# Kernel optimization log

Measured on AMD Instinct MI355X. Metric: run time of the kernel, lower is better.

The kernel has to match this reference:

```python
import jax, jax.numpy as jnp
import numpy as np

N_IN, N_OUT = 8192, 4096
INIT_TAU = 2.0
V_TH = 1.0
SLOPE = 10.0  # fast-sigmoid surrogate slope


def setup_inputs() -> dict:
    key = jax.random.key(0)
    k1, k2, k3, k4, k5 = jax.random.split(key, 5)
    x = jax.random.normal(k1, (N_IN,), jnp.float32)
    W = jax.random.normal(k2, (N_IN, N_OUT), jnp.float32) / np.sqrt(N_IN).astype(np.float32)
    u = jax.random.normal(k3, (N_OUT,), jnp.float32)
    E = jax.random.normal(k4, (N_IN, N_OUT), jnp.float32) * 0.1
    R_hat = jax.random.normal(k5, (N_IN, N_OUT), jnp.float32) * 0.1
    g_bar = jnp.zeros((N_OUT,), jnp.float32)
    ratio = jnp.zeros((1,), jnp.float32)
    return {"x": x, "W": W, "u": u, "E": E, "R_hat": R_hat, "g_bar": g_bar, "ratio": ratio}


def _step(x, W, u, E, R_hat, g_bar, ratio):
    # One OTPE timestep. SNN: Dense connection + LIF with soft (detached) reset.
    sig_tau = jax.nn.sigmoid(jnp.float32(INIT_TAU))
    u_pre = sig_tau * u + x @ W                       # [n_out]
    s = (u_pre >= V_TH).astype(jnp.float32)           # spike (heaviside fwd)
    sg = 1.0 / (1.0 + SLOPE * jnp.abs(u_pre - V_TH)) ** 2  # surrogate d s/d u_pre
    u_new = u_pre - s * V_TH                          # soft reset (s detached)
    # analytic per-step VJPs of sum(s) and sum(u) wrt (u_prev, theta):
    ds_du_prev = sg * sig_tau                         # [n_out]
    ds_dtheta_cur = x[:, None] * sg[None, :]          # [n_in, n_out]
    # du_cur_du_prev = sig_tau ; du_cur_dtheta_cur = outer(x, ones)
    ds_dtheta = ds_du_prev[None, :] * E + ds_dtheta_cur   # map_s over pytree
    E_new = sig_tau * E + x[:, None]                      # map_u over pytree
    R_new = sig_tau * R_hat + ds_dtheta                   # map_r
    r0 = sig_tau * ratio                               # [1]
    ratio_new = r0 + 1.0
    r = r0 / ratio_new
    g_bar_new = r * g_bar + (1.0 - r) * (ds_du_prev / sig_tau)
    return s, u_new, E_new, R_new, g_bar_new, ratio_new


def reference(x, W, u, E, R_hat, g_bar, ratio):
    # returns (s, carry_u, carry_E, carry_R_hat, carry_g_bar, carry_ratio)
    return _step(x, W, u, E, R_hat, g_bar, ratio)
```

## Files before the change

kernel.cpp:

```cpp
#include <hip/hip_runtime.h>


#define SIG_TAU 0.8807970779778823f

typedef float f32x4 __attribute__((ext_vector_type(4)));

constexpr int N_IN  = 8192;
constexpr int N_OUT = 4096;
constexpr int NCG   = N_OUT / 4;
constexpr int NCHUNK = 256;
constexpr int ROWS_PER_CHUNK = N_IN / NCHUNK;
constexpr int ROWS_PER_CHUNK_ATOM = 64;

constexpr size_t OFF_S     = 0;
constexpr size_t OFF_U     = (size_t)N_OUT;
constexpr size_t OFF_E     = (size_t)2 * N_OUT;
constexpr size_t OFF_R     = OFF_E + (size_t)N_IN * N_OUT;
constexpr size_t OFF_G     = OFF_R + (size_t)N_IN * N_OUT;
constexpr size_t OFF_RATIO = OFF_G + (size_t)N_OUT;

__global__ __launch_bounds__(256) void matvec_split(
    const float* __restrict__ x, const f32x4* __restrict__ W4,
    f32x4* __restrict__ part4) {
    const int cg    = blockIdx.x * 256 + threadIdx.x;
    const int chunk = blockIdx.y;
    const int row0  = chunk * ROWS_PER_CHUNK;
    f32x4 a = {0.f, 0.f, 0.f, 0.f};
#pragma unroll 8
    for (int r = 0; r < ROWS_PER_CHUNK; ++r) {
        const float xv = x[row0 + r];
        const f32x4 w  = __builtin_nontemporal_load(
            &W4[(size_t)(row0 + r) * NCG + cg]);
        a[0] = fmaf(xv, w[0], a[0]);
        a[1] = fmaf(xv, w[1], a[1]);
        a[2] = fmaf(xv, w[2], a[2]);
        a[3] = fmaf(xv, w[3], a[3]);
    }
    part4[(size_t)chunk * NCG + cg] = a;
}

__global__ __launch_bounds__(256) void matvec_atomic(
    const float* __restrict__ x, const f32x4* __restrict__ W4,
    float* __restrict__ acc) {
    const int cg   = blockIdx.x * 256 + threadIdx.x;
    const int row0 = blockIdx.y * ROWS_PER_CHUNK_ATOM;
    f32x4 a = {0.f, 0.f, 0.f, 0.f};
#pragma unroll 8
    for (int r = 0; r < ROWS_PER_CHUNK_ATOM; ++r) {
        const float xv = x[row0 + r];
        const f32x4 w  = W4[(size_t)(row0 + r) * NCG + cg];
        a[0] = fmaf(xv, w[0], a[0]);
        a[1] = fmaf(xv, w[1], a[1]);
        a[2] = fmaf(xv, w[2], a[2]);
        a[3] = fmaf(xv, w[3], a[3]);
    }
    float* dst = acc + (size_t)cg * 4;
    atomicAdd(dst + 0, a[0]);
    atomicAdd(dst + 1, a[1]);
    atomicAdd(dst + 2, a[2]);
    atomicAdd(dst + 3, a[3]);
}

__global__ __launch_bounds__(256) void finalize(
    const float* __restrict__ part, const int nchunks,
    const float* __restrict__ u, const float* __restrict__ g_bar,
    const float* __restrict__ ratio, float* __restrict__ out,
    float* __restrict__ sg_ws) {
    const int j = blockIdx.x * 256 + threadIdx.x;
    if (j >= N_OUT) return;
    float acc = 0.f;
#pragma unroll 8
    for (int c = 0; c < nchunks; ++c)
        acc += part[(size_t)c * N_OUT + j];

    const float u_pre = fmaf(SIG_TAU, u[j], acc);
    const float s     = (u_pre >= 1.0f) ? 1.0f : 0.0f;
    const float t     = 1.0f / fmaf(10.0f, fabsf(u_pre - 1.0f), 1.0f);
    const float sg    = t * t;
    const float u_new = u_pre - s;

    const float r0        = SIG_TAU * ratio[0];
    const float ratio_new = r0 + 1.0f;
    const float r         = r0 / ratio_new;
    const float g_new = fmaf(r, g_bar[j], (1.0f - r) * sg);

    out[OFF_S + j] = s;
    out[OFF_U + j] = u_new;
    out[OFF_G + j] = g_new;
    sg_ws[j] = sg;
    if (j == 0) out[OFF_RATIO] = ratio_new;
}

__global__ __launch_bounds__(256) void elemwise(
    const float* __restrict__ x, const f32x4* __restrict__ E4,
    const f32x4* __restrict__ R4, const f32x4* __restrict__ sg4,
    f32x4* __restrict__ Enew4, f32x4* __restrict__ Rnew4) {
    const int tid = threadIdx.x;
    const f32x4 s0 = sg4[tid];
    const f32x4 s1 = sg4[tid + 256];
    const f32x4 s2 = sg4[tid + 512];
    const f32x4 s3 = sg4[tid + 768];

    for (int row = blockIdx.x; row < N_IN; row += gridDim.x) {
        const float  xv   = x[row];
        const size_t base = (size_t)row * NCG + tid;

        const f32x4 e0 = E4[base];
        const f32x4 e1 = E4[base + 256];
        const f32x4 e2 = E4[base + 512];
        const f32x4 e3 = E4[base + 768];
        const f32x4 r0 = R4[base];
        const f32x4 r1 = R4[base + 256];
        const f32x4 r2 = R4[base + 512];
        const f32x4 r3 = R4[base + 768];

        f32x4 en0, en1, en2, en3, rn0, rn1, rn2, rn3;
#define COMP(k)                                                   \
        en##k[0] = fmaf(SIG_TAU, e##k[0], xv);                    \
        en##k[1] = fmaf(SIG_TAU, e##k[1], xv);                    \
        en##k[2] = fmaf(SIG_TAU, e##k[2], xv);                    \
        en##k[3] = fmaf(SIG_TAU, e##k[3], xv);                    \
        rn##k[0] = fmaf(s##k[0], en##k[0], SIG_TAU * r##k[0]);    \
        rn##k[1] = fmaf(s##k[1], en##k[1], SIG_TAU * r##k[1]);    \
        rn##k[2] = fmaf(s##k[2], en##k[2], SIG_TAU * r##k[2]);    \
        rn##k[3] = fmaf(s##k[3], en##k[3], SIG_TAU * r##k[3]);
        COMP(0) COMP(1) COMP(2) COMP(3)
#undef COMP

        Enew4[base]       = en0;
        Enew4[base + 256] = en1;
        Enew4[base + 512] = en2;
        Enew4[base + 768] = en3;
        Rnew4[base]       = rn0;
        Rnew4[base + 256] = rn1;
        Rnew4[base + 512] = rn2;
        Rnew4[base + 768] = rn3;
    }
}

extern "C" void kernel_launch(void* const* d_in, const int* in_sizes, int n_in,
                              void* d_out, int out_size, void* d_ws, size_t ws_size,
                              hipStream_t stream) {
    const float* x     = (const float*)d_in[0];
    const float* W     = (const float*)d_in[1];
    const float* u     = (const float*)d_in[2];
    const float* E     = (const float*)d_in[3];
    const float* R_hat = (const float*)d_in[4];
    const float* g_bar = (const float*)d_in[5];
    const float* ratio = (const float*)d_in[6];
    float* out = (float*)d_out;

    float* sg   = (float*)d_ws;
    float* part = sg + N_OUT;

    const size_t need = (size_t)(N_OUT + (size_t)NCHUNK * N_OUT) * sizeof(float);
    if (ws_size >= need) {
        dim3 g1(NCG / 256, NCHUNK);
        matvec_split<<<g1, 256, 0, stream>>>(x, (const f32x4*)W, (f32x4*)part);
        finalize<<<N_OUT / 256, 256, 0, stream>>>(
            part, NCHUNK, u, g_bar, ratio, out, sg);
    } else {
        hipMemsetAsync(part, 0, N_OUT * sizeof(float), stream);
        dim3 g1(NCG / 256, N_IN / ROWS_PER_CHUNK_ATOM);
        matvec_atomic<<<g1, 256, 0, stream>>>(x, (const f32x4*)W, part);
        finalize<<<N_OUT / 256, 256, 0, stream>>>(
            part, 1, u, g_bar, ratio, out, sg);
    }

    elemwise<<<2048, 256, 0, stream>>>(
        x, (const f32x4*)E, (const f32x4*)R_hat, (const f32x4*)sg,
        (f32x4*)(out + OFF_E), (f32x4*)(out + OFF_R));
}
```

Baseline: 538.7 us.

## Split elementwise kernel into E update before finalize and R update after

Splits the fused E/R update into two kernels: E_new is computed right after the matvec, before finalize, since it does not depend on the surrogate gradient. The R kernel then reads E_new back from the output instead of recomputing it. Nontemporal loads and stores are added on the streaming arrays. This adds an extra full-size read of E_new and relies on same-stream ordering, so no true overlap is gained.

Measured after the change: 530.2 us. No clear change (-1.6%).

```diff
diff --git a/kernel.cpp b/kernel.cpp
--- a/kernel.cpp
+++ b/kernel.cpp
@@ -91,50 +91,62 @@
     if (j == 0) out[OFF_RATIO] = ratio_new;
 }
 
-__global__ __launch_bounds__(256) void elemwise(
+__global__ __launch_bounds__(256) void ew_E(
     const float* __restrict__ x, const f32x4* __restrict__ E4,
-    const f32x4* __restrict__ R4, const f32x4* __restrict__ sg4,
-    f32x4* __restrict__ Enew4, f32x4* __restrict__ Rnew4) {
+    f32x4* __restrict__ Enew4) {
+    const int tid = threadIdx.x;
+    for (int row = blockIdx.x; row < N_IN; row += gridDim.x) {
+        const float  xv   = x[row];
+        const size_t base = (size_t)row * NCG + tid;
+        const f32x4 e0 = __builtin_nontemporal_load(&E4[base]);
+        const f32x4 e1 = __builtin_nontemporal_load(&E4[base + 256]);
+        const f32x4 e2 = __builtin_nontemporal_load(&E4[base + 512]);
+        const f32x4 e3 = __builtin_nontemporal_load(&E4[base + 768]);
+        f32x4 en0, en1, en2, en3;
+#define CE(k)                                      \
+        en##k[0] = fmaf(SIG_TAU, e##k[0], xv);     \
+        en##k[1] = fmaf(SIG_TAU, e##k[1], xv);     \
+        en##k[2] = fmaf(SIG_TAU, e##k[2], xv);     \
+        en##k[3] = fmaf(SIG_TAU, e##k[3], xv);
+        CE(0) CE(1) CE(2) CE(3)
+#undef CE
+        Enew4[base]       = en0;
+        Enew4[base + 256] = en1;
+        Enew4[base + 512] = en2;
+        Enew4[base + 768] = en3;
+    }
+}
+
+__global__ __launch_bounds__(256) void ew_R(
+    const f32x4* __restrict__ R4, const f32x4* __restrict__ Enew4,
+    const f32x4* __restrict__ sg4, f32x4* __restrict__ Rnew4) {
     const int tid = threadIdx.x;
     const f32x4 s0 = sg4[tid];
     const f32x4 s1 = sg4[tid + 256];
     const f32x4 s2 = sg4[tid + 512];
     const f32x4 s3 = sg4[tid + 768];
-
     for (int row = blockIdx.x; row < N_IN; row += gridDim.x) {
-        const float  xv   = x[row];
         const size_t base = (size_t)row * NCG + tid;
-
-        const f32x4 e0 = E4[base];
-        const f32x4 e1 = E4[base + 256];
-        const f32x4 e2 = E4[base + 512];
-        const f32x4 e3 = E4[base + 768];
-        const f32x4 r0 = R4[base];
-        const f32x4 r1 = R4[base + 256];
-        const f32x4 r2 = R4[base + 512];
-        const f32x4 r3 = R4[base + 768];
-
-        f32x4 en0, en1, en2, en3, rn0, rn1, rn2, rn3;
-#define COMP(k)                                                   \
-        en##k[0] = fmaf(SIG_TAU, e##k[0], xv);                    \
-        en##k[1] = fmaf(SIG_TAU, e##k[1], xv);                    \
-        en##k[2] = fmaf(SIG_TAU, e##k[2], xv);                    \
-        en##k[3] = fmaf(SIG_TAU, e##k[3], xv);                    \
+        const f32x4 r0 = __builtin_nontemporal_load(&R4[base]);
+        const f32x4 r1 = __builtin_nontemporal_load(&R4[base + 256]);
+        const f32x4 r2 = __builtin_nontemporal_load(&R4[base + 512]);
+        const f32x4 r3 = __builtin_nontemporal_load(&R4[base + 768]);
+        const f32x4 en0 = Enew4[base];
+        const f32x4 en1 = Enew4[base + 256];
+        const f32x4 en2 = Enew4[base + 512];
+        const f32x4 en3 = Enew4[base + 768];
+        f32x4 rn0, rn1, rn2, rn3;
+#define CR(k)                                                     \
         rn##k[0] = fmaf(s##k[0], en##k[0], SIG_TAU * r##k[0]);    \
         rn##k[1] = fmaf(s##k[1], en##k[1], SIG_TAU * r##k[1]);    \
         rn##k[2] = fmaf(s##k[2], en##k[2], SIG_TAU * r##k[2]);    \
         rn##k[3] = fmaf(s##k[3], en##k[3], SIG_TAU * r##k[3]);
-        COMP(0) COMP(1) COMP(2) COMP(3)
-#undef COMP
-
-        Enew4[base]       = en0;
-        Enew4[base + 256] = en1;
-        Enew4[base + 512] = en2;
-        Enew4[base + 768] = en3;
-        Rnew4[base]       = rn0;
-        Rnew4[base + 256] = rn1;
-        Rnew4[base + 512] = rn2;
-        Rnew4[base + 768] = rn3;
+        CR(0) CR(1) CR(2) CR(3)
+#undef CR
+        __builtin_nontemporal_store(rn0, &Rnew4[base]);
+        __builtin_nontemporal_store(rn1, &Rnew4[base + 256]);
+        __builtin_nontemporal_store(rn2, &Rnew4[base + 512]);
+        __builtin_nontemporal_store(rn3, &Rnew4[base + 768]);
     }
 }
 
@@ -153,21 +165,25 @@
     float* sg   = (float*)d_ws;
     float* part = sg + N_OUT;
 
+    f32x4* Enew4 = (f32x4*)(out + OFF_E);
+    f32x4* Rnew4 = (f32x4*)(out + OFF_R);
+
     const size_t need = (size_t)(N_OUT + (size_t)NCHUNK * N_OUT) * sizeof(float);
     if (ws_size >= need) {
         dim3 g1(NCG / 256, NCHUNK);
         matvec_split<<<g1, 256, 0, stream>>>(x, (const f32x4*)W, (f32x4*)part);
+        ew_E<<<2048, 256, 0, stream>>>(x, (const f32x4*)E, Enew4);
         finalize<<<N_OUT / 256, 256, 0, stream>>>(
             part, NCHUNK, u, g_bar, ratio, out, sg);
     } else {
         hipMemsetAsync(part, 0, N_OUT * sizeof(float), stream);
         dim3 g1(NCG / 256, N_IN / ROWS_PER_CHUNK_ATOM);
         matvec_atomic<<<g1, 256, 0, stream>>>(x, (const f32x4*)W, part);
+        ew_E<<<2048, 256, 0, stream>>>(x, (const f32x4*)E, Enew4);
         finalize<<<N_OUT / 256, 256, 0, stream>>>(
             part, 1, u, g_bar, ratio, out, sg);
     }
 
-    elemwise<<<2048, 256, 0, stream>>>(
-        x, (const f32x4*)E, (const f32x4*)R_hat, (const f32x4*)sg,
-        (f32x4*)(out + OFF_E), (f32x4*)(out + OFF_R));
+    ew_R<<<2048, 256, 0, stream>>>(
+        (const f32x4*)R_hat, (const f32x4*)Enew4, (const f32x4*)sg, Rnew4);
 }
```

## Fuse matvec, finalize and elementwise into one cooperative kernel with grid syncs

Applied to the files above, without the earlier changes.

Adds a cooperative megakernel that runs the split-K matvec, the per-output finalize and the E/R elementwise update as three phases separated by grid.sync(). The goal is to remove two kernel launch boundaries and the idle gaps between them. The W loads also drop their nontemporal hint, and the elementwise phase now uses 1024 blocks instead of 2048. In exchange it pays two grid-wide barriers, leaves most blocks idle during the 16-block finalize phase, and needs the cooperative grid to fit fully resident. The old atomic fallback is replaced by a path that launches matvec_split over a single chunk, so it would only sum the first rows when the workspace is small.

Result: slower. 760.3 us (+41.1%).

```diff
diff --git a/kernel.cpp b/kernel.cpp
--- a/kernel.cpp
+++ b/kernel.cpp
@@ -1,4 +1,7 @@
 #include <hip/hip_runtime.h>
+#include <hip/hip_cooperative_groups.h>
+
+namespace cg = cooperative_groups;
 
 
 #define SIG_TAU 0.8807970779778823f
@@ -11,6 +14,7 @@
 constexpr int NCHUNK = 256;
 constexpr int ROWS_PER_CHUNK = N_IN / NCHUNK;
 constexpr int ROWS_PER_CHUNK_ATOM = 64;
+constexpr int MEGA_GRID = 1024;
 
 constexpr size_t OFF_S     = 0;
 constexpr size_t OFF_U     = (size_t)N_OUT;
@@ -18,6 +22,110 @@
 constexpr size_t OFF_R     = OFF_E + (size_t)N_IN * N_OUT;
 constexpr size_t OFF_G     = OFF_R + (size_t)N_IN * N_OUT;
 constexpr size_t OFF_RATIO = OFF_G + (size_t)N_OUT;
+
+__global__ __launch_bounds__(256, 4) void otpe_mega(
+    const float* __restrict__ x, const f32x4* __restrict__ W4,
+    const float* __restrict__ u, const f32x4* __restrict__ E4,
+    const f32x4* __restrict__ R4, const float* __restrict__ g_bar,
+    const float* __restrict__ ratio, float* __restrict__ out,
+    float* __restrict__ sg_ws, f32x4* __restrict__ part4) {
+    cg::grid_group grid = cg::this_grid();
+    const int tid = threadIdx.x;
+    const int bid = blockIdx.x;
+
+    {
+        const int cgi   = (bid & 3) * 256 + tid;
+        const int chunk = bid >> 2;
+        const int row0  = chunk * ROWS_PER_CHUNK;
+        f32x4 a = {0.f, 0.f, 0.f, 0.f};
+#pragma unroll 8
+        for (int r = 0; r < ROWS_PER_CHUNK; ++r) {
+            const float xv = x[row0 + r];
+            const f32x4 w  = W4[(size_t)(row0 + r) * NCG + cgi];
+            a[0] = fmaf(xv, w[0], a[0]);
+            a[1] = fmaf(xv, w[1], a[1]);
+            a[2] = fmaf(xv, w[2], a[2]);
+            a[3] = fmaf(xv, w[3], a[3]);
+        }
+        part4[(size_t)chunk * NCG + cgi] = a;
+    }
+
+    grid.sync();
+
+    if (bid < 16) {
+        const int j = bid * 256 + tid;
+        const float* part = (const float*)part4;
+        float acc = 0.f;
+#pragma unroll 8
+        for (int c = 0; c < NCHUNK; ++c)
+            acc += part[(size_t)c * N_OUT + j];
+
+        const float u_pre = fmaf(SIG_TAU, u[j], acc);
+        const float s     = (u_pre >= 1.0f) ? 1.0f : 0.0f;
+        const float t     = 1.0f / fmaf(10.0f, fabsf(u_pre - 1.0f), 1.0f);
+        const float sg    = t * t;
+        const float u_new = u_pre - s;
+
+        const float r0        = SIG_TAU * ratio[0];
+        const float ratio_new = r0 + 1.0f;
+        const float r         = r0 / ratio_new;
+        const float g_new = fmaf(r, g_bar[j], (1.0f - r) * sg);
+
+        out[OFF_S + j] = s;
+        out[OFF_U + j] = u_new;
+        out[OFF_G + j] = g_new;
+        sg_ws[j] = sg;
+        if (j == 0) out[OFF_RATIO] = ratio_new;
+    }
+
+    grid.sync();
+
+    {
+        f32x4* Enew4 = (f32x4*)(out + OFF_E);
+        f32x4* Rnew4 = (f32x4*)(out + OFF_R);
+        const f32x4* sg4 = (const f32x4*)sg_ws;
+        const f32x4 s0 = sg4[tid];
+        const f32x4 s1 = sg4[tid + 256];
+        const f32x4 s2 = sg4[tid + 512];
+        const f32x4 s3 = sg4[tid + 768];
+
+        for (int row = bid; row < N_IN; row += MEGA_GRID) {
+            const float  xv   = x[row];
+            const size_t base = (size_t)row * NCG + tid;
+
+            const f32x4 e0 = E4[base];
+            const f32x4 e1 = E4[base + 256];
+            const f32x4 e2 = E4[base + 512];
+            const f32x4 e3 = E4[base + 768];
+            const f32x4 r0 = R4[base];
+            const f32x4 r1 = R4[base + 256];
+            const f32x4 r2 = R4[base + 512];
+            const f32x4 r3 = R4[base + 768];
+
+            f32x4 en0, en1, en2, en3, rn0, rn1, rn2, rn3;
+#define COMP(k)                                                   \
+            en##k[0] = fmaf(SIG_TAU, e##k[0], xv);                \
+            en##k[1] = fmaf(SIG_TAU, e##k[1], xv);                \
+            en##k[2] = fmaf(SIG_TAU, e##k[2], xv);                \
+            en##k[3] = fmaf(SIG_TAU, e##k[3], xv);                \
+            rn##k[0] = fmaf(s##k[0], en##k[0], SIG_TAU * r##k[0]);\
+            rn##k[1] = fmaf(s##k[1], en##k[1], SIG_TAU * r##k[1]);\
+            rn##k[2] = fmaf(s##k[2], en##k[2], SIG_TAU * r##k[2]);\
+            rn##k[3] = fmaf(s##k[3], en##k[3], SIG_TAU * r##k[3]);
+            COMP(0) COMP(1) COMP(2) COMP(3)
+#undef COMP
+
+            Enew4[base]       = en0;
+            Enew4[base + 256] = en1;
+            Enew4[base + 512] = en2;
+            Enew4[base + 768] = en3;
+            Rnew4[base]       = rn0;
+            Rnew4[base + 256] = rn1;
+            Rnew4[base + 512] = rn2;
+            Rnew4[base + 768] = rn3;
+        }
+    }
+}
 
 __global__ __launch_bounds__(256) void matvec_split(
     const float* __restrict__ x, const f32x4* __restrict__ W4,
@@ -29,36 +137,13 @@
 #pragma unroll 8
     for (int r = 0; r < ROWS_PER_CHUNK; ++r) {
         const float xv = x[row0 + r];
-        const f32x4 w  = __builtin_nontemporal_load(
-            &W4[(size_t)(row0 + r) * NCG + cg]);
-        a[0] = fmaf(xv, w[0], a[0]);
-        a[1] = fmaf(xv, w[1], a[1]);
-        a[2] = fmaf(xv, w[2], a[2]);
-        a[3] = fmaf(xv, w[3], a[3]);
-    }
-    part4[(size_t)chunk * NCG + cg] = a;
-}
-
-__global__ __launch_bounds__(256) void matvec_atomic(
-    const float* __restrict__ x, const f32x4* __restrict__ W4,
-    float* __restrict__ acc) {
-    const int cg   = blockIdx.x * 256 + threadIdx.x;
-    const int row0 = blockIdx.y * ROWS_PER_CHUNK_ATOM;
-    f32x4 a = {0.f, 0.f, 0.f, 0.f};
-#pragma unroll 8
-    for (int r = 0; r < ROWS_PER_CHUNK_ATOM; ++r) {
-        const float xv = x[row0 + r];
         const f32x4 w  = W4[(size_t)(row0 + r) * NCG + cg];
         a[0] = fmaf(xv, w[0], a[0]);
         a[1] = fmaf(xv, w[1], a[1]);
         a[2] = fmaf(xv, w[2], a[2]);
         a[3] = fmaf(xv, w[3], a[3]);
     }
-    float* dst = acc + (size_t)cg * 4;
-    atomicAdd(dst + 0, a[0]);
-    atomicAdd(dst + 1, a[1]);
-    atomicAdd(dst + 2, a[2]);
-    atomicAdd(dst + 3, a[3]);
+    part4[(size_t)chunk * NCG + cg] = a;
 }
 
 __global__ __launch_bounds__(256) void finalize(
@@ -91,7 +176,7 @@
     if (j == 0) out[OFF_RATIO] = ratio_new;
 }
 
-__global__ __launch_bounds__(256) void elemwise(
+__global__ __launch_bounds__(256) void ew_fused(
     const float* __restrict__ x, const f32x4* __restrict__ E4,
     const f32x4* __restrict__ R4, const f32x4* __restrict__ sg4,
     f32x4* __restrict__ Enew4, f32x4* __restrict__ Rnew4) {
@@ -100,11 +185,9 @@
     const f32x4 s1 = sg4[tid + 256];
     const f32x4 s2 = sg4[tid + 512];
     const f32x4 s3 = sg4[tid + 768];
-
     for (int row = blockIdx.x; row < N_IN; row += gridDim.x) {
         const float  xv   = x[row];
         const size_t base = (size_t)row * NCG + tid;
-
         const f32x4 e0 = E4[base];
         const f32x4 e1 = E4[base + 256];
         const f32x4 e2 = E4[base + 512];
@@ -113,7 +196,6 @@
         const f32x4 r1 = R4[base + 256];
         const f32x4 r2 = R4[base + 512];
         const f32x4 r3 = R4[base + 768];
-
         f32x4 en0, en1, en2, en3, rn0, rn1, rn2, rn3;
 #define COMP(k)                                                   \
         en##k[0] = fmaf(SIG_TAU, e##k[0], xv);                    \
@@ -126,7 +208,6 @@
         rn##k[3] = fmaf(s##k[3], en##k[3], SIG_TAU * r##k[3]);
         COMP(0) COMP(1) COMP(2) COMP(3)
 #undef COMP
-
         Enew4[base]       = en0;
         Enew4[base + 256] = en1;
         Enew4[base + 512] = en2;
@@ -153,21 +234,46 @@
     float* sg   = (float*)d_ws;
     float* part = sg + N_OUT;
 
+    const f32x4* W4p = (const f32x4*)W;
+    const f32x4* E4p = (const f32x4*)E;
+    const f32x4* R4p = (const f32x4*)R_hat;
+    f32x4*       part4p = (f32x4*)part;
+    f32x4*       Enew4  = (f32x4*)(out + OFF_E);
+    f32x4*       Rnew4  = (f32x4*)(out + OFF_R);
+    const f32x4* sg4p   = (const f32x4*)sg;
+
     const size_t need = (size_t)(N_OUT + (size_t)NCHUNK * N_OUT) * sizeof(float);
+    bool done = false;
+
     if (ws_size >= need) {
-        dim3 g1(NCG / 256, NCHUNK);
-        matvec_split<<<g1, 256, 0, stream>>>(x, (const f32x4*)W, (f32x4*)part);
-        finalize<<<N_OUT / 256, 256, 0, stream>>>(
-            part, NCHUNK, u, g_bar, ratio, out, sg);
-    } else {
-        hipMemsetAsync(part, 0, N_OUT * sizeof(float), stream);
-        dim3 g1(NCG / 256, N_IN / ROWS_PER_CHUNK_ATOM);
-        matvec_atomic<<<g1, 256, 0, stream>>>(x, (const f32x4*)W, part);
+        int dev = 0, coop = 0;
+        hipGetDevice(&dev);
+        hipDeviceGetAttribute(&coop, hipDeviceAttributeCooperativeLaunch, dev);
+        if (coop) {
+            void* args[] = {
+                (void*)&x, (void*)&W4p, (void*)&u, (void*)&E4p, (void*)&R4p,
+                (void*)&g_bar, (void*)&ratio, (void*)&out, (void*)&sg,
+                (void*)&part4p};
+            hipError_t e = hipLaunchCooperativeKernel(
+                (const void*)otpe_mega, dim3(MEGA_GRID), dim3(256), args, 0,
+                stream);
+            done = (e == hipSuccess);
+        }
+        if (!done) {
+            dim3 g1(NCG / 256, NCHUNK);
+            matvec_split<<<g1, 256, 0, stream>>>(x, W4p, part4p);
+            finalize<<<N_OUT / 256, 256, 0, stream>>>(
+                part, NCHUNK, u, g_bar, ratio, out, sg);
+            ew_fused<<<2048, 256, 0, stream>>>(x, E4p, R4p, sg4p, Enew4, Rnew4);
+            done = true;
+        }
+    }
+
+    if (!done) {
+        dim3 g1(NCG / 256, 1);
+        matvec_split<<<g1, 256, 0, stream>>>(x, W4p, part4p);
         finalize<<<N_OUT / 256, 256, 0, stream>>>(
             part, 1, u, g_bar, ratio, out, sg);
-    }
-
-    elemwise<<<2048, 256, 0, stream>>>(
-        x, (const f32x4*)E, (const f32x4*)R_hat, (const f32x4*)sg,
-        (f32x4*)(out + OFF_E), (f32x4*)(out + OFF_R));
-}
+        ew_fused<<<2048, 256, 0, stream>>>(x, E4p, R4p, sg4p, Enew4, Rnew4);
+    }
+}
```
